# Kernel optimization log

Measured on AMD Instinct MI355X. Metric: run time of the kernel, lower is better.

## Reference

```python
import jax, jax.numpy as jnp
import numpy as np

N = 100000   # num_nodes
D = 128      # hidden_dim
E = 640000   # num_edges


def setup_inputs() -> dict:
    key = jax.random.key(0)
    k0, k1, k2, k3 = jax.random.split(key, 4)
    node_features = jax.random.normal(k0, (N, D), dtype=jnp.float32) * 0.02
    # GCNConv linear weights (glorot-style scale), bias initialized to zero
    scale = 1.0 / np.sqrt(D)
    W1 = jax.random.normal(k1, (D, D), dtype=jnp.float32) * scale
    b1 = jnp.zeros((D,), dtype=jnp.float32)
    W2 = jax.random.normal(k2, (D, D), dtype=jnp.float32) * scale
    b2 = jnp.zeros((D,), dtype=jnp.float32)
    edge_index = jax.random.randint(k3, (2, E), 0, N, dtype=jnp.int32)
    return {"node_features": node_features, "W1": W1, "b1": b1,
            "W2": W2, "b2": b2, "edge_index": edge_index}


def gcn_layer(x, W, b, row, col):
    # PyG GCNConv: linear (no bias) -> symmetric norm deg^-1/2 -> scatter-add -> +bias
    x = x @ W.T                                   # [N, D]
    ones = jnp.ones(row.shape, dtype=x.dtype)
    deg = jax.ops.segment_sum(ones, col, num_segments=N)   # in-degree incl. self-loops
    dis = jnp.where(deg > 0, jax.lax.rsqrt(deg), 0.0)       # deg_inv_sqrt, inf -> 0
    norm = dis[row] * dis[col]                    # [E_tot]
    msgs = norm[:, None] * x[row]                 # gather + scale, [E_tot, D]
    out = jax.ops.segment_sum(msgs, col, num_segments=N)    # scatter-aggregate
    return out + b


def reference(node_features, W1, b1, W2, b2, edge_index):
    # add self-loops once (GCNConv does this per call; same result since graph is static)
    loops = jnp.arange(N, dtype=edge_index.dtype)
    row = jnp.concatenate([edge_index[0], loops])
    col = jnp.concatenate([edge_index[1], loops])
    x = jax.nn.relu(gcn_layer(node_features, W1, b1, row, col))
    x = jax.nn.relu(gcn_layer(x, W2, b2, row, col))
    return x
```

## Files before the change

kernel.cpp:

```cpp
#include <hip/hip_runtime.h>

#define DD 128

typedef short bf16x8 __attribute__((ext_vector_type(8)));
typedef float f32x4 __attribute__((ext_vector_type(4)));

__device__ __forceinline__ unsigned short f2bf(float f) {
    unsigned int u = __builtin_bit_cast(unsigned int, f);
    u += 0x7fffu + ((u >> 16) & 1u);
    return (unsigned short)(u >> 16);
}
__device__ __forceinline__ float bflo(unsigned int u) { return __builtin_bit_cast(float, u << 16); }
__device__ __forceinline__ float bfhi(unsigned int u) { return __builtin_bit_cast(float, u & 0xffff0000u); }

__global__ __launch_bounds__(256) void k_part(const int* __restrict__ cnt,
                                              int* __restrict__ part, int n) {
    __shared__ int s[256];
    int t = threadIdx.x;
    int i = blockIdx.x * 256 + t;
    s[t] = (i < n) ? cnt[i] : 0;
    __syncthreads();
    for (int off = 128; off > 0; off >>= 1) {
        if (t < off) s[t] += s[t + off];
        __syncthreads();
    }
    if (t == 0) part[blockIdx.x] = s[0];
}

__global__ __launch_bounds__(1024) void k_scanpart(int* __restrict__ part, int nblk) {
    __shared__ int s[1024];
    int t = threadIdx.x;
    int v = (t < nblk) ? part[t] : 0;
    s[t] = v;
    __syncthreads();
    for (int off = 1; off < 1024; off <<= 1) {
        int u = (t >= off) ? s[t - off] : 0;
        __syncthreads();
        s[t] += u;
        __syncthreads();
    }
    if (t < nblk) part[t] = s[t] - v;
}

__global__ __launch_bounds__(256) void k_apply(const int* __restrict__ cnt,
                                               const int* __restrict__ part,
                                               int* __restrict__ rowptr,
                                               int* __restrict__ cursor,
                                               float* __restrict__ dis, int n) {
    __shared__ int s[256];
    int t = threadIdx.x;
    int i = blockIdx.x * 256 + t;
    int c = (i < n) ? cnt[i] : 0;
    s[t] = c;
    __syncthreads();
    for (int off = 1; off < 256; off <<= 1) {
        int u = (t >= off) ? s[t - off] : 0;
        __syncthreads();
        s[t] += u;
        __syncthreads();
    }
    int base = part[blockIdx.x] + s[t] - c;
    if (i < n) {
        rowptr[i] = base;
        cursor[i] = base;
        dis[i] = rsqrtf((float)c + 1.0f);
        if (i == n - 1) rowptr[n] = base + c;
    }
}

__global__ void k_permute(const int* __restrict__ row, const int* __restrict__ col,
                          int* __restrict__ cursor, int* __restrict__ srow, int E) {
    int e = blockIdx.x * blockDim.x + threadIdx.x;
    if (e >= E) return;
    int p = atomicAdd(&cursor[col[e]], 1);
    srow[p] = row[e];
}

template <bool INBF16, bool FUSE_COUNT>
__global__ __launch_bounds__(512) void k_gemm_mfma(const void* __restrict__ Xv,
                                                   const float* __restrict__ W,
                                                   unsigned short* __restrict__ Y,
                                                   int nrows, int gemm_blocks,
                                                   const int* __restrict__ col,
                                                   int* __restrict__ cnt, int E) {
    __shared__ unsigned short Ws[128 * 128];
    const int t = threadIdx.x;

    if (FUSE_COUNT && blockIdx.x >= gemm_blocks) {
        int e = (blockIdx.x - gemm_blocks) * 512 + t;
        if (e < E) atomicAdd(&cnt[col[e]], 1);
        return;
    }

    #pragma unroll
    for (int i = 0; i < 4; ++i) {
        int g   = i * 512 + t;
        int row = g >> 4, ch = g & 15;
        const float* src = W + row * 128 + ch * 8;
        float4 f0 = *(const float4*)src;
        float4 f1 = *(const float4*)(src + 4);
        unsigned short u[8] = { f2bf(f0.x), f2bf(f0.y), f2bf(f0.z), f2bf(f0.w),
                                f2bf(f1.x), f2bf(f1.y), f2bf(f1.z), f2bf(f1.w) };
        int dst = row * 128 + ((ch ^ (row & 15)) << 3);
        *(uint4*)&Ws[dst] = *(const uint4*)u;
    }
    __syncthreads();

    const int wid  = t >> 6;
    const int lane = t & 63;
    const int lr   = lane & 15;
    const int lk   = lane >> 4;
    const long r0  = (long)blockIdx.x * 128 + wid * 16;

    long arow = r0 + lr;
    bool rowok = arow < nrows;
    if (!rowok) arow = nrows - 1;

    f32x4 acc[8] = {};

    #pragma unroll
    for (int kc = 0; kc < 4; ++kc) {
        bf16x8 af;
        if (INBF16) {
            const unsigned short* ap = (const unsigned short*)Xv + arow * 128 + kc * 32 + lk * 8;
            af = *(const bf16x8*)ap;
        } else {
            const float* ap = (const float*)Xv + arow * 128 + kc * 32 + lk * 8;
            float4 a0 = *(const float4*)ap;
            float4 a1 = *(const float4*)(ap + 4);
            af[0] = (short)f2bf(a0.x); af[1] = (short)f2bf(a0.y);
            af[2] = (short)f2bf(a0.z); af[3] = (short)f2bf(a0.w);
            af[4] = (short)f2bf(a1.x); af[5] = (short)f2bf(a1.y);
            af[6] = (short)f2bf(a1.z); af[7] = (short)f2bf(a1.w);
        }
        #pragma unroll
        for (int jt = 0; jt < 8; ++jt) {
            int j  = jt * 16 + lr;
            int ch = (kc * 4 + lk) ^ lr;
            const bf16x8* bp = (const bf16x8*)&Ws[j * 128 + (ch << 3)];
            acc[jt] = __builtin_amdgcn_mfma_f32_16x16x32_bf16(*bp, af, acc[jt], 0, 0, 0);
        }
    }

    if (rowok) {
        unsigned short* yp = Y + arow * 128 + lk * 4;
        #pragma unroll
        for (int jt = 0; jt < 8; ++jt) {
            unsigned int d0 = (unsigned int)f2bf(acc[jt][0]) | ((unsigned int)f2bf(acc[jt][1]) << 16);
            unsigned int d1 = (unsigned int)f2bf(acc[jt][2]) | ((unsigned int)f2bf(acc[jt][3]) << 16);
            uint2 u; u.x = d0; u.y = d1;
            *(uint2*)(yp + jt * 16) = u;
        }
    }
}

__device__ __forceinline__ void fma8(float* acc, float nm, uint4 q) {
    acc[0] += nm * bflo(q.x); acc[1] += nm * bfhi(q.x);
    acc[2] += nm * bflo(q.y); acc[3] += nm * bfhi(q.y);
    acc[4] += nm * bflo(q.z); acc[5] += nm * bfhi(q.z);
    acc[6] += nm * bflo(q.w); acc[7] += nm * bfhi(q.w);
}

template <bool OUTBF16>
__global__ __launch_bounds__(256) void k_agg(const int* __restrict__ rowptr,
                                             const int* __restrict__ srow,
                                             const float* __restrict__ dis,
                                             const unsigned short* __restrict__ xw,
                                             const float* __restrict__ b,
                                             void* __restrict__ outv, int n) {
    int v = blockIdx.x * 16 + (threadIdx.x >> 4);
    if (v >= n) return;
    int c = (threadIdx.x & 15) * 8;

    float dv = dis[v], s = dv * dv;
    float acc[8] = {};
    fma8(acc, s, *(const uint4*)(xw + (long)v * 128 + c));

    int e0 = rowptr[v], e1 = rowptr[v + 1];
    int e = e0;
    for (; e + 4 <= e1; e += 4) {
        int   r1 = srow[e],     r2 = srow[e + 1];
        int   r3 = srow[e + 2], r4 = srow[e + 3];
        float n1 = dis[r1] * dv, n2 = dis[r2] * dv;
        float n3 = dis[r3] * dv, n4 = dis[r4] * dv;
        uint4 q1 = *(const uint4*)(xw + (long)r1 * 128 + c);
        uint4 q2 = *(const uint4*)(xw + (long)r2 * 128 + c);
        uint4 q3 = *(const uint4*)(xw + (long)r3 * 128 + c);
        uint4 q4 = *(const uint4*)(xw + (long)r4 * 128 + c);
        fma8(acc, n1, q1);
        fma8(acc, n2, q2);
        fma8(acc, n3, q3);
        fma8(acc, n4, q4);
    }
    for (; e < e1; ++e) {
        int   r1 = srow[e];
        float n1 = dis[r1] * dv;
        fma8(acc, n1, *(const uint4*)(xw + (long)r1 * 128 + c));
    }

    float4 b0 = *(const float4*)(b + c);
    float4 b1 = *(const float4*)(b + c + 4);
    float o[8];
    o[0] = fmaxf(acc[0] + b0.x, 0.0f); o[1] = fmaxf(acc[1] + b0.y, 0.0f);
    o[2] = fmaxf(acc[2] + b0.z, 0.0f); o[3] = fmaxf(acc[3] + b0.w, 0.0f);
    o[4] = fmaxf(acc[4] + b1.x, 0.0f); o[5] = fmaxf(acc[5] + b1.y, 0.0f);
    o[6] = fmaxf(acc[6] + b1.z, 0.0f); o[7] = fmaxf(acc[7] + b1.w, 0.0f);

    if (OUTBF16) {
        unsigned int p[4];
        p[0] = (unsigned int)f2bf(o[0]) | ((unsigned int)f2bf(o[1]) << 16);
        p[1] = (unsigned int)f2bf(o[2]) | ((unsigned int)f2bf(o[3]) << 16);
        p[2] = (unsigned int)f2bf(o[4]) | ((unsigned int)f2bf(o[5]) << 16);
        p[3] = (unsigned int)f2bf(o[6]) | ((unsigned int)f2bf(o[7]) << 16);
        *(uint4*)((unsigned short*)outv + (long)v * 128 + c) = *(const uint4*)p;
    } else {
        float* op = (float*)outv + (long)v * 128 + c;
        *(float4*)op       = make_float4(o[0], o[1], o[2], o[3]);
        *(float4*)(op + 4) = make_float4(o[4], o[5], o[6], o[7]);
    }
}

extern "C" void kernel_launch(void* const* d_in, const int* in_sizes, int n_in,
                              void* d_out, int out_size, void* d_ws, size_t ws_size,
                              hipStream_t stream) {
    const float* X  = (const float*)d_in[0];
    const float* W1 = (const float*)d_in[1];
    const float* b1 = (const float*)d_in[2];
    const float* W2 = (const float*)d_in[3];
    const float* b2 = (const float*)d_in[4];
    const int*   ei = (const int*)d_in[5];
    const int N = in_sizes[0] / DD;
    const int E = in_sizes[5] / 2;
    const int* row = ei;
    const int* col = ei + E;

    char* p = (char*)d_ws;
    auto carve = [&](size_t bytes) { char* q = p; p += (bytes + 255) & ~(size_t)255; return q; };
    int*            cnt    = (int*)           carve((size_t)N * 4);
    int*            rowptr = (int*)           carve((size_t)(N + 1) * 4);
    int*            cursor = (int*)           carve((size_t)N * 4);
    int*            part   = (int*)           carve(1024 * 4);
    int*            srow   = (int*)           carve((size_t)E * 4);
    float*          dis    = (float*)         carve((size_t)N * 4);
    unsigned short* xw     = (unsigned short*)carve((size_t)N * DD * 2);
    unsigned short* h1     = (unsigned short*)d_out;

    const int NBLK = (N + 255) / 256;
    const int gemm_grid  = (N + 127) / 128;
    const int count_grid = (E + 511) / 512;
    const int perm_grid  = (E + 255) / 256;
    const int agg_grid   = (N + 15) / 16;

    hipMemsetAsync(cnt, 0, (size_t)N * 4, stream);
    k_gemm_mfma<false, true><<<gemm_grid + count_grid, 512, 0, stream>>>(
        X, W1, xw, N, gemm_grid, col, cnt, E);

    k_part<<<NBLK, 256, 0, stream>>>(cnt, part, N);
    k_scanpart<<<1, 1024, 0, stream>>>(part, NBLK);
    k_apply<<<NBLK, 256, 0, stream>>>(cnt, part, rowptr, cursor, dis, N);
    k_permute<<<perm_grid, 256, 0, stream>>>(row, col, cursor, srow, E);

    k_agg<true><<<agg_grid, 256, 0, stream>>>(rowptr, srow, dis, xw, b1, h1, N);

    k_gemm_mfma<true, false><<<gemm_grid, 512, 0, stream>>>(
        h1, W2, xw, N, gemm_grid, nullptr, nullptr, 0);
    k_agg<false><<<agg_grid, 256, 0, stream>>>(rowptr, srow, dis, xw, b2, d_out, N);
}
```

Baseline: 174.4 us.

## Fuse edge permutation into first GEMM and stage GEMM output through LDS

The edge-count pass moves into its own kernel, and the permute (scatter of row indices into CSR order) is folded into the first GEMM launch as extra blocks. The permute's atomic scatter can then overlap with the MFMA work instead of running as a separate launch. The GEMM epilogue now writes results into shared memory with a swizzle and copies them out as full 16-byte row-contiguous stores, replacing the scattered 8-byte stores. This adds two block barriers, and the count kernel becomes a standalone launch that no longer overlaps with the GEMM.

```diff
diff --git a/kernel.cpp b/kernel.cpp
--- a/kernel.cpp
+++ b/kernel.cpp
@@ -12,6 +12,12 @@
 }
 __device__ __forceinline__ float bflo(unsigned int u) { return __builtin_bit_cast(float, u << 16); }
 __device__ __forceinline__ float bfhi(unsigned int u) { return __builtin_bit_cast(float, u & 0xffff0000u); }
+
+__global__ __launch_bounds__(512) void k_count(const int* __restrict__ col,
+                                               int* __restrict__ cnt, int E) {
+    int e = blockIdx.x * 512 + threadIdx.x;
+    if (e < E) atomicAdd(&cnt[col[e]], 1);
+}
 
 __global__ __launch_bounds__(256) void k_part(const int* __restrict__ cnt,
                                               int* __restrict__ part, int n) {
@@ -68,40 +74,37 @@
     }
 }
 
-__global__ void k_permute(const int* __restrict__ row, const int* __restrict__ col,
-                          int* __restrict__ cursor, int* __restrict__ srow, int E) {
-    int e = blockIdx.x * blockDim.x + threadIdx.x;
-    if (e >= E) return;
-    int p = atomicAdd(&cursor[col[e]], 1);
-    srow[p] = row[e];
-}
-
-template <bool INBF16, bool FUSE_COUNT>
+template <bool INBF16, bool FUSE_PERM>
 __global__ __launch_bounds__(512) void k_gemm_mfma(const void* __restrict__ Xv,
                                                    const float* __restrict__ W,
                                                    unsigned short* __restrict__ Y,
                                                    int nrows, int gemm_blocks,
-                                                   const int* __restrict__ col,
-                                                   int* __restrict__ cnt, int E) {
+                                                   const int* __restrict__ erow,
+                                                   const int* __restrict__ ecol,
+                                                   int* __restrict__ cursor,
+                                                   int* __restrict__ srow, int E) {
     __shared__ unsigned short Ws[128 * 128];
     const int t = threadIdx.x;
 
-    if (FUSE_COUNT && blockIdx.x >= gemm_blocks) {
+    if (FUSE_PERM && blockIdx.x >= gemm_blocks) {
         int e = (blockIdx.x - gemm_blocks) * 512 + t;
-        if (e < E) atomicAdd(&cnt[col[e]], 1);
+        if (e < E) {
+            int p = atomicAdd(&cursor[ecol[e]], 1);
+            srow[p] = erow[e];
+        }
         return;
     }
 
     #pragma unroll
     for (int i = 0; i < 4; ++i) {
-        int g   = i * 512 + t;
-        int row = g >> 4, ch = g & 15;
-        const float* src = W + row * 128 + ch * 8;
+        int g  = i * 512 + t;
+        int wr = g >> 4, ch = g & 15;
+        const float* src = W + wr * 128 + ch * 8;
         float4 f0 = *(const float4*)src;
         float4 f1 = *(const float4*)(src + 4);
         unsigned short u[8] = { f2bf(f0.x), f2bf(f0.y), f2bf(f0.z), f2bf(f0.w),
                                 f2bf(f1.x), f2bf(f1.y), f2bf(f1.z), f2bf(f1.w) };
-        int dst = row * 128 + ((ch ^ (row & 15)) << 3);
+        int dst = wr * 128 + ((ch ^ (wr & 15)) << 3);
         *(uint4*)&Ws[dst] = *(const uint4*)u;
     }
     __syncthreads();
@@ -110,11 +113,11 @@
     const int lane = t & 63;
     const int lr   = lane & 15;
     const int lk   = lane >> 4;
-    const long r0  = (long)blockIdx.x * 128 + wid * 16;
-
-    long arow = r0 + lr;
-    bool rowok = arow < nrows;
-    if (!rowok) arow = nrows - 1;
+    const int wrow = wid * 16 + lr;
+    const long base = (long)blockIdx.x * 128;
+
+    long arow = base + wrow;
+    if (arow >= nrows) arow = nrows - 1;
 
     f32x4 acc[8] = {};
 
@@ -142,14 +145,25 @@
         }
     }
 
-    if (rowok) {
-        unsigned short* yp = Y + arow * 128 + lk * 4;
-        #pragma unroll
-        for (int jt = 0; jt < 8; ++jt) {
-            unsigned int d0 = (unsigned int)f2bf(acc[jt][0]) | ((unsigned int)f2bf(acc[jt][1]) << 16);
-            unsigned int d1 = (unsigned int)f2bf(acc[jt][2]) | ((unsigned int)f2bf(acc[jt][3]) << 16);
-            uint2 u; u.x = d0; u.y = d1;
-            *(uint2*)(yp + jt * 16) = u;
+    __syncthreads();
+    #pragma unroll
+    for (int jt = 0; jt < 8; ++jt) {
+        unsigned int d0 = (unsigned int)f2bf(acc[jt][0]) | ((unsigned int)f2bf(acc[jt][1]) << 16);
+        unsigned int d1 = (unsigned int)f2bf(acc[jt][2]) | ((unsigned int)f2bf(acc[jt][3]) << 16);
+        int cc16 = jt * 2 + (lk >> 1);
+        int half = lk & 1;
+        uint2 u; u.x = d0; u.y = d1;
+        *(uint2*)&Ws[wrow * 128 + ((cc16 ^ lr) << 3) + half * 4] = u;
+    }
+    __syncthreads();
+    #pragma unroll
+    for (int p = 0; p < 4; ++p) {
+        int r    = p * 32 + (t >> 4);
+        int cc16 = t & 15;
+        long grow = base + r;
+        if (grow < nrows) {
+            uint4 v = *(const uint4*)&Ws[r * 128 + ((cc16 ^ (r & 15)) << 3)];
+            *(uint4*)(Y + grow * 128 + cc16 * 8) = v;
         }
     }
 }
@@ -207,12 +221,12 @@
     o[6] = fmaxf(acc[6] + b1.z, 0.0f); o[7] = fmaxf(acc[7] + b1.w, 0.0f);
 
     if (OUTBF16) {
-        unsigned int p[4];
-        p[0] = (unsigned int)f2bf(o[0]) | ((unsigned int)f2bf(o[1]) << 16);
-        p[1] = (unsigned int)f2bf(o[2]) | ((unsigned int)f2bf(o[3]) << 16);
-        p[2] = (unsigned int)f2bf(o[4]) | ((unsigned int)f2bf(o[5]) << 16);
-        p[3] = (unsigned int)f2bf(o[6]) | ((unsigned int)f2bf(o[7]) << 16);
-        *(uint4*)((unsigned short*)outv + (long)v * 128 + c) = *(const uint4*)p;
+        unsigned int pk[4];
+        pk[0] = (unsigned int)f2bf(o[0]) | ((unsigned int)f2bf(o[1]) << 16);
+        pk[1] = (unsigned int)f2bf(o[2]) | ((unsigned int)f2bf(o[3]) << 16);
+        pk[2] = (unsigned int)f2bf(o[4]) | ((unsigned int)f2bf(o[5]) << 16);
+        pk[3] = (unsigned int)f2bf(o[6]) | ((unsigned int)f2bf(o[7]) << 16);
+        *(uint4*)((unsigned short*)outv + (long)v * 128 + c) = *(const uint4*)pk;
     } else {
         float* op = (float*)outv + (long)v * 128 + c;
         *(float4*)op       = make_float4(o[0], o[1], o[2], o[3]);
@@ -247,22 +261,21 @@
 
     const int NBLK = (N + 255) / 256;
     const int gemm_grid  = (N + 127) / 128;
-    const int count_grid = (E + 511) / 512;
-    const int perm_grid  = (E + 255) / 256;
+    const int edge_grid  = (E + 511) / 512;
     const int agg_grid   = (N + 15) / 16;
 
     hipMemsetAsync(cnt, 0, (size_t)N * 4, stream);
-    k_gemm_mfma<false, true><<<gemm_grid + count_grid, 512, 0, stream>>>(
-        X, W1, xw, N, gemm_grid, col, cnt, E);
-
+    k_count<<<edge_grid, 512, 0, stream>>>(col, cnt, E);
     k_part<<<NBLK, 256, 0, stream>>>(cnt, part, N);
     k_scanpart<<<1, 1024, 0, stream>>>(part, NBLK);
     k_apply<<<NBLK, 256, 0, stream>>>(cnt, part, rowptr, cursor, dis, N);
-    k_permute<<<perm_grid, 256, 0, stream>>>(row, col, cursor, srow, E);
+
+    k_gemm_mfma<false, true><<<gemm_grid + edge_grid, 512, 0, stream>>>(
+        X, W1, xw, N, gemm_grid, row, col, cursor, srow, E);
 
     k_agg<true><<<agg_grid, 256, 0, stream>>>(rowptr, srow, dis, xw, b1, h1, N);
 
     k_gemm_mfma<true, false><<<gemm_grid, 512, 0, stream>>>(
-        h1, W2, xw, N, gemm_grid, nullptr, nullptr, 0);
+        h1, W2, xw, N, gemm_grid, nullptr, nullptr, nullptr, nullptr, 0);
     k_agg<false><<<agg_grid, 256, 0, stream>>>(rowptr, srow, dis, xw, b2, d_out, N);
 }
```

New measurement: 176.7 us. Within noise of the previous version (+1.3%).
